# Kernel tuning notes

Hardware: AMD Instinct MI355X
Metric: run time of the kernel (lower is better)

Reference implementation:

```python
import jax, jax.numpy as jnp
import numpy as np

N, P, C, H, W, M = 2, 3, 80, 64, 64, 524288
HID = 64
BOX_WARP = 2.0


def _linear_init(key, fan_in, fan_out):
    # kaiming-uniform-ish; bias is zero-init per the torch module
    bound = 1.0 / np.sqrt(fan_in)
    return jax.random.uniform(key, (fan_in, fan_out), jnp.float32, -bound, bound)


def setup_inputs() -> dict:
    key = jax.random.key(0)
    ks = jax.random.split(key, 6)
    planes = jax.random.normal(ks[0], (N, P, C, H, W), jnp.float32)
    coordinates = jax.random.uniform(ks[1], (N, M, 3), jnp.float32, -1.0, 1.0)
    W1 = _linear_init(ks[2], 3 * C, HID)
    W2 = _linear_init(ks[3], HID, HID)
    W3 = _linear_init(ks[4], HID, HID)
    W4 = _linear_init(ks[5], HID, 1)
    return {
        "planes": planes, "coordinates": coordinates,
        "W1": W1, "b1": jnp.zeros((HID,), jnp.float32),
        "W2": W2, "b2": jnp.zeros((HID,), jnp.float32),
        "W3": W3, "b3": jnp.zeros((HID,), jnp.float32),
        "W4": W4, "b4": jnp.zeros((1,), jnp.float32),
    }


def _grid_sample_bilinear(feat, grid):
    # feat: [B, C, H, W]; grid: [B, M, 2] in [-1, 1] (x, y order),
    # bilinear, padding_mode='zeros', align_corners=False (matches torch).
    B, Cc, Hh, Ww = feat.shape
    gx = (grid[..., 0] + 1.0) * (Ww * 0.5) - 0.5  # [B, M]
    gy = (grid[..., 1] + 1.0) * (Hh * 0.5) - 0.5
    x0 = jnp.floor(gx)
    y0 = jnp.floor(gy)
    wx1 = gx - x0
    wy1 = gy - y0
    featf = feat.transpose(0, 2, 3, 1).reshape(B, Hh * Ww, Cc)  # [B, HW, C]

    def gather(xi, yi):
        valid = (xi >= 0) & (xi < Ww) & (yi >= 0) & (yi < Hh)
        xc = jnp.clip(xi, 0, Ww - 1).astype(jnp.int32)
        yc = jnp.clip(yi, 0, Hh - 1).astype(jnp.int32)
        idx = yc * Ww + xc  # [B, M]
        v = jnp.take_along_axis(featf, idx[..., None], axis=1)  # [B, M, C]
        return v * valid[..., None].astype(feat.dtype)

    v00 = gather(x0, y0)
    v01 = gather(x0 + 1, y0)
    v10 = gather(x0, y0 + 1)
    v11 = gather(x0 + 1, y0 + 1)
    wx1 = wx1[..., None]
    wy1 = wy1[..., None]
    top = v00 * (1.0 - wx1) + v01 * wx1
    bot = v10 * (1.0 - wx1) + v11 * wx1
    return top * (1.0 - wy1) + bot * wy1  # [B, M, C]


def _plane_axes():
    return jnp.array(
        [[[1, 0, 0], [0, 1, 0], [0, 0, 1]],
         [[1, 0, 0], [0, 0, 1], [0, 1, 0]],
         [[0, 0, 1], [0, 1, 0], [1, 0, 0]]], jnp.float32)


def reference(planes, coordinates, W1, b1, W2, b2, W3, b3, W4, b4):
    n, p, c, h, w = planes.shape
    m = coordinates.shape[1]
    inv_axes = jnp.linalg.inv(_plane_axes())  # [3, 3, 3]
    coords = (2.0 / BOX_WARP) * coordinates  # [N, M, 3]
    # project: coords @ inv_plane per plane, keep first two coords
    proj = jnp.einsum('nmc,pcd->npmd', coords, inv_axes)[..., :2]  # [N, P, M, 2]
    feat = planes.reshape(n * p, c, h, w)
    grid = proj.reshape(n * p, m, 2)
    samp = _grid_sample_bilinear(feat, grid)  # [N*P, M, C]
    # [N, P, M, C] -> [N, M, P*C]
    x = samp.reshape(n, p, m, c).transpose(0, 2, 1, 3).reshape(n, m, p * c)
    hdn = jax.nn.relu(x @ W1 + b1)
    hdn = jax.nn.relu(hdn @ W2 + b2)
    hdn = jax.nn.relu(hdn @ W3 + b3)
    sdf = hdn @ W4 + b4  # [N, M, 1]
    return sdf
```

## Files before the change

kernel.cpp:

```cpp
#include <hip/hip_runtime.h>
#include <hip/hip_bf16.h>
#include <stdint.h>

#define MPTS  524288
#define NB    2
#define CCH   80
#define HWDIM 64
#define HID   64

typedef _Float16 f16x2 __attribute__((ext_vector_type(2)));
typedef _Float16 f16x8 __attribute__((ext_vector_type(8)));
typedef float    f32x4 __attribute__((ext_vector_type(4)));

union FragH { uint4 q; f16x8 v; f16x2 h2[4]; _Float16 h[8]; };

__device__ __forceinline__ void fma_mix_lo(float& acc, unsigned u, float w) {
    asm volatile("v_fma_mix_f32 %0, %1, %2, %0 op_sel_hi:[1,0,0]"
                 : "+v"(acc) : "v"(u), "v"(w));
}
__device__ __forceinline__ void fma_mix_hi(float& acc, unsigned u, float w) {
    asm volatile("v_fma_mix_f32 %0, %1, %2, %0 op_sel:[1,0,0] op_sel_hi:[1,0,0]"
                 : "+v"(acc) : "v"(u), "v"(w));
}

__global__ void precompute_planesW(const float* __restrict__ planes,
                                   const float* __restrict__ W1,
                                   unsigned short* __restrict__ planesW) {
    __shared__ float tA[CCH * 64];
    __shared__ float tW[CCH * 64];
    int b  = blockIdx.x;
    int np = b >> 6, y = b & 63;
    int p  = np % 3;
    int t  = threadIdx.x;
    for (int i = t; i < CCH * 64; i += 256) {
        int c = i >> 6, x = i & 63;
        tA[i] = planes[((size_t)np * CCH + c) * 4096 + y * 64 + x];
        tW[i] = W1[(p * CCH + c) * HID + x];
    }
    __syncthreads();
    int px = t >> 2;
    int n0 = (t & 3) * 16;
    float acc[16];
    #pragma unroll
    for (int i = 0; i < 16; ++i) acc[i] = 0.0f;
    for (int c = 0; c < CCH; ++c) {
        float a = tA[c * 64 + px];
        #pragma unroll
        for (int i = 0; i < 16; ++i) acc[i] += a * tW[c * 64 + n0 + i];
    }
    unsigned short* dst = planesW + (((size_t)np * 4096) + y * 64 + px) * HID + n0;
    #pragma unroll
    for (int i = 0; i < 16; ++i) {
        union { _Float16 h; unsigned short u; } cv;
        cv.h = (_Float16)acc[i];
        dst[i] = cv.u;
    }
}

__global__ void pack_weights23(const float* __restrict__ W2,
                               const float* __restrict__ W3,
                               unsigned short* __restrict__ wpack) {
    int e = blockIdx.x * 256 + threadIdx.x;
    const float* W = (e < 4096) ? W2 : W3;
    int q  = e & 4095;
    int j  = q & 7;
    int l  = (q >> 3) & 63;
    int nt = (q >> 9) & 3;
    int kb = q >> 11;
    int k  = kb * 32 + ((l >> 4) << 3) + j;
    int nn = nt * 16 + (l & 15);
    union { _Float16 h; unsigned short u; } cv;
    cv.h = (_Float16)W[k * HID + nn];
    wpack[e] = cv.u;
}

__global__ __launch_bounds__(256, 4) void fused_kernel(
        const unsigned short* __restrict__ planesW,
        const float* __restrict__ coords,
        const unsigned short* __restrict__ wpack,
        const float* __restrict__ b1, const float* __restrict__ b2,
        const float* __restrict__ b3, const float* __restrict__ W4,
        const float* __restrict__ b4, float* __restrict__ out) {

    __shared__ __align__(16) unsigned short sH[4 * 16 * 72];
    __shared__ __align__(16) uint4 sSet[64][3][2];

    int t    = threadIdx.x;
    int wave = t >> 6, lane = t & 63;
    int ptbase = blockIdx.x * 64 + wave * 16;

    unsigned short* hw = sH + wave * (16 * 72);
    _Float16* hwh = (_Float16*)hw;

    if (t < 192) {
        int i  = t & 63;
        int p  = t >> 6;
        int mypt = blockIdx.x * 64 + i;
        int n    = mypt >> 19;
        const float* cp = coords + (size_t)mypt * 3;
        float c0 = cp[0], c1 = cp[1], c2 = cp[2];
        float gx = (p == 2) ? c2 : c0;
        float gy = (p == 1) ? c2 : c1;
        float fx = (gx + 1.0f) * 32.0f - 0.5f;
        float fy = (gy + 1.0f) * 32.0f - 0.5f;
        float xf = floorf(fx), yf = floorf(fy);
        float wx = fx - xf,    wy = fy - yf;
        int x0 = (int)xf, y0 = (int)yf, x1 = x0 + 1, y1 = y0 + 1;
        float vx0 = (x0 >= 0 && x0 < 64) ? 1.0f : 0.0f;
        float vx1 = (x1 >= 0 && x1 < 64) ? 1.0f : 0.0f;
        float vy0 = (y0 >= 0 && y0 < 64) ? 1.0f : 0.0f;
        float vy1 = (y1 >= 0 && y1 < 64) ? 1.0f : 0.0f;
        int cx0 = min(max(x0, 0), 63), cx1 = min(max(x1, 0), 63);
        int cy0 = min(max(y0, 0), 63), cy1 = min(max(y1, 0), 63);
        union { float f[4]; uint4 q; } wq;
        wq.f[0] = (1.0f - wx) * (1.0f - wy) * vx0 * vy0;
        wq.f[1] = wx * (1.0f - wy) * vx1 * vy0;
        wq.f[2] = (1.0f - wx) * wy * vx0 * vy1;
        wq.f[3] = wx * wy * vx1 * vy1;
        int base = (n * 3 + p) * 4096;
        uint4 oq;
        oq.x = (unsigned)((base + (cy0 << 6) + cx0) * HID);
        oq.y = (unsigned)((base + (cy0 << 6) + cx1) * HID);
        oq.z = (unsigned)((base + (cy1 << 6) + cx0) * HID);
        oq.w = (unsigned)((base + (cy1 << 6) + cx1) * HID);
        sSet[i][p][0] = oq;
        sSet[i][p][1] = wq.q;
    }
    __syncthreads();

    {
        int sub = lane & 7;
        int ptg = lane >> 3;

        float b1f0, b1f1, b1f2, b1f3, b1f4, b1f5, b1f6, b1f7;
        {
            const float4* bp = (const float4*)(b1 + sub * 8);
            float4 v0 = bp[0], v1 = bp[1];
            b1f0 = v0.x; b1f1 = v0.y; b1f2 = v0.z; b1f3 = v0.w;
            b1f4 = v1.x; b1f5 = v1.y; b1f6 = v1.z; b1f7 = v1.w;
        }
        const unsigned short* pw = planesW + sub * 8;

        auto do_round = [&](int pt) {
            int pl = wave * 16 + pt;
            uint4 o0 = sSet[pl][0][0], w0c = sSet[pl][0][1];
            uint4 o1 = sSet[pl][1][0], w1c = sSet[pl][1][1];
            uint4 o2 = sSet[pl][2][0], w2c = sSet[pl][2][1];

            FragH u0, u1, u2, u3, u4, u5, u6, u7, u8, u9, u10, u11;
            u0.q  = *(const uint4*)(pw + o0.x);
            u1.q  = *(const uint4*)(pw + o0.y);
            u2.q  = *(const uint4*)(pw + o0.z);
            u3.q  = *(const uint4*)(pw + o0.w);
            u4.q  = *(const uint4*)(pw + o1.x);
            u5.q  = *(const uint4*)(pw + o1.y);
            u6.q  = *(const uint4*)(pw + o1.z);
            u7.q  = *(const uint4*)(pw + o1.w);
            u8.q  = *(const uint4*)(pw + o2.x);
            u9.q  = *(const uint4*)(pw + o2.y);
            u10.q = *(const uint4*)(pw + o2.z);
            u11.q = *(const uint4*)(pw + o2.w);

            float a0 = b1f0, a1 = b1f1, a2 = b1f2, a3 = b1f3;
            float a4 = b1f4, a5 = b1f5, a6 = b1f6, a7 = b1f7;
            union { unsigned u; float f; } cvu;

            #define TEXEL(T, WB) { cvu.u = (WB); float w = cvu.f;            \
                fma_mix_lo(a0, T.q.x, w); fma_mix_hi(a1, T.q.x, w);          \
                fma_mix_lo(a2, T.q.y, w); fma_mix_hi(a3, T.q.y, w);          \
                fma_mix_lo(a4, T.q.z, w); fma_mix_hi(a5, T.q.z, w);          \
                fma_mix_lo(a6, T.q.w, w); fma_mix_hi(a7, T.q.w, w); }
            TEXEL(u0,  w0c.x) TEXEL(u1,  w0c.y) TEXEL(u2,  w0c.z) TEXEL(u3,  w0c.w)
            TEXEL(u4,  w1c.x) TEXEL(u5,  w1c.y) TEXEL(u6,  w1c.z) TEXEL(u7,  w1c.w)
            TEXEL(u8,  w2c.x) TEXEL(u9,  w2c.y) TEXEL(u10, w2c.z) TEXEL(u11, w2c.w)
            #undef TEXEL

            FragH hv;
            hv.h[0] = (_Float16)fmaxf(a0, 0.0f);
            hv.h[1] = (_Float16)fmaxf(a1, 0.0f);
            hv.h[2] = (_Float16)fmaxf(a2, 0.0f);
            hv.h[3] = (_Float16)fmaxf(a3, 0.0f);
            hv.h[4] = (_Float16)fmaxf(a4, 0.0f);
            hv.h[5] = (_Float16)fmaxf(a5, 0.0f);
            hv.h[6] = (_Float16)fmaxf(a6, 0.0f);
            hv.h[7] = (_Float16)fmaxf(a7, 0.0f);
            *(uint4*)(hwh + pt * 72 + sub * 8) = hv.q;
        };
        do_round(ptg);
        do_round(8 + ptg);
    }
    __syncthreads();

    int row  = lane & 15;
    int kgrp = lane >> 4;
    f32x4 acc2[4] = {{0,0,0,0},{0,0,0,0},{0,0,0,0},{0,0,0,0}};
    #pragma unroll
    for (int kk = 0; kk < 2; ++kk) {
        FragH au;
        au.q = *(const uint4*)(hw + row * 72 + kk * 32 + kgrp * 8);
        #pragma unroll
        for (int nt = 0; nt < 4; ++nt) {
            FragH bu;
            bu.q = *(const uint4*)(wpack + (kk * 4 + nt) * 512 + lane * 8);
            acc2[nt] = __builtin_amdgcn_mfma_f32_16x16x32_f16(au.v, bu.v, acc2[nt], 0, 0, 0);
        }
    }
    __syncthreads();

    #pragma unroll
    for (int nt = 0; nt < 4; ++nt) {
        float bb = b2[nt * 16 + row];
        #pragma unroll
        for (int r = 0; r < 4; ++r) {
            float h = fmaxf(acc2[nt][r] + bb, 0.0f);
            hwh[(kgrp * 4 + r) * 72 + nt * 16 + row] = (_Float16)h;
        }
    }
    __syncthreads();

    f32x4 acc3[4] = {{0,0,0,0},{0,0,0,0},{0,0,0,0},{0,0,0,0}};
    #pragma unroll
    for (int kk = 0; kk < 2; ++kk) {
        FragH au;
        au.q = *(const uint4*)(hw + row * 72 + kk * 32 + kgrp * 8);
        #pragma unroll
        for (int nt = 0; nt < 4; ++nt) {
            FragH bu;
            bu.q = *(const uint4*)(wpack + 4096 + (kk * 4 + nt) * 512 + lane * 8);
            acc3[nt] = __builtin_amdgcn_mfma_f32_16x16x32_f16(au.v, bu.v, acc3[nt], 0, 0, 0);
        }
    }

    float part[4] = {0.f, 0.f, 0.f, 0.f};
    #pragma unroll
    for (int nt = 0; nt < 4; ++nt) {
        float bb  = b3[nt * 16 + row];
        float w4v = W4[nt * 16 + row];
        #pragma unroll
        for (int r = 0; r < 4; ++r) {
            float h = fmaxf(acc3[nt][r] + bb, 0.0f);
            part[r] += h * w4v;
        }
    }
    #pragma unroll
    for (int r = 0; r < 4; ++r) {
        #pragma unroll
        for (int off = 1; off < 16; off <<= 1)
            part[r] += __shfl_xor(part[r], off);
    }
    if (row == 0) {
        float bias4 = b4[0];
        float4 o;
        o.x = part[0] + bias4; o.y = part[1] + bias4;
        o.z = part[2] + bias4; o.w = part[3] + bias4;
        *(float4*)(out + ptbase + kgrp * 4) = o;
    }
}

extern "C" void kernel_launch(void* const* d_in, const int* in_sizes, int n_in,
                              void* d_out, int out_size, void* d_ws, size_t ws_size,
                              hipStream_t stream) {
    const float* planes = (const float*)d_in[0];
    const float* coords = (const float*)d_in[1];
    const float* W1 = (const float*)d_in[2];
    const float* b1 = (const float*)d_in[3];
    const float* W2 = (const float*)d_in[4];
    const float* b2 = (const float*)d_in[5];
    const float* W3 = (const float*)d_in[6];
    const float* b3 = (const float*)d_in[7];
    const float* W4 = (const float*)d_in[8];
    const float* b4 = (const float*)d_in[9];
    float* out = (float*)d_out;

    unsigned short* planesW = (unsigned short*)d_ws;
    unsigned short* wpack   = (unsigned short*)((char*)d_ws + 3145728);

    hipLaunchKernelGGL(precompute_planesW, dim3(NB * 3 * HWDIM), dim3(256), 0, stream,
                       planes, W1, planesW);
    hipLaunchKernelGGL(pack_weights23, dim3(32), dim3(256), 0, stream,
                       W2, W3, wpack);

    int nblocks = (NB * MPTS) / 64;
    hipLaunchKernelGGL(fused_kernel, dim3(nblocks), dim3(256), 0, stream,
                       planesW, coords, wpack, b1, b2, b3, W4, b4, out);
}
```

Before: 108.4 us.

## Sort points into spatial cells before fused gather-MLP kernel for cache locality

Adds a counting sort of the 1M query points into 16x16x16 spatial cells per batch (histogram with atomics, single-block scan, atomic scatter into a permutation). The fused kernel reads points through the permutation and scatters outputs back to their original positions. The aim is for nearby points in a block to gather nearby texels of the precomputed plane features, improving L2/L1 hit rates. The cost is three extra kernels plus a memset, atomic contention, and scattered 4-byte output stores instead of float4 stores.

```diff
diff --git a/kernel.cpp b/kernel.cpp
--- a/kernel.cpp
+++ b/kernel.cpp
@@ -7,6 +7,8 @@
 #define CCH   80
 #define HWDIM 64
 #define HID   64
+#define NPTS  (NB * MPTS)
+#define NCELL 8192
 
 typedef _Float16 f16x2 __attribute__((ext_vector_type(2)));
 typedef _Float16 f16x8 __attribute__((ext_vector_type(8)));
@@ -21,6 +23,50 @@
 __device__ __forceinline__ void fma_mix_hi(float& acc, unsigned u, float w) {
     asm volatile("v_fma_mix_f32 %0, %1, %2, %0 op_sel:[1,0,0] op_sel_hi:[1,0,0]"
                  : "+v"(acc) : "v"(u), "v"(w));
+}
+
+__device__ __forceinline__ int cell_key(const float* __restrict__ coords, int idx) {
+    const float* cp = coords + (size_t)idx * 3;
+    int cx = min(max((int)((cp[0] + 1.0f) * 8.0f), 0), 15);
+    int cy = min(max((int)((cp[1] + 1.0f) * 8.0f), 0), 15);
+    int cz = min(max((int)((cp[2] + 1.0f) * 8.0f), 0), 15);
+    return ((idx >> 19) << 12) | (cx << 8) | (cy << 4) | cz;
+}
+
+__global__ void hist_kernel(const float* __restrict__ coords,
+                            unsigned* __restrict__ hist) {
+    int idx = blockIdx.x * 256 + threadIdx.x;
+    if (idx >= NPTS) return;
+    atomicAdd(&hist[cell_key(coords, idx)], 1u);
+}
+
+__global__ __launch_bounds__(1024) void scan_kernel(unsigned* __restrict__ hist) {
+    __shared__ unsigned s[1024];
+    int t = threadIdx.x;
+    unsigned v[8], pre[8], sum = 0;
+    #pragma unroll
+    for (int j = 0; j < 8; ++j) { v[j] = hist[t * 8 + j]; pre[j] = sum; sum += v[j]; }
+    s[t] = sum;
+    __syncthreads();
+    for (int off = 1; off < 1024; off <<= 1) {
+        unsigned x = 0;
+        if (t >= off) x = s[t - off];
+        __syncthreads();
+        if (t >= off) s[t] += x;
+        __syncthreads();
+    }
+    unsigned base = (t > 0) ? s[t - 1] : 0u;
+    #pragma unroll
+    for (int j = 0; j < 8; ++j) hist[t * 8 + j] = base + pre[j];
+}
+
+__global__ void scatter_kernel(const float* __restrict__ coords,
+                               unsigned* __restrict__ cursor,
+                               unsigned* __restrict__ perm) {
+    int idx = blockIdx.x * 256 + threadIdx.x;
+    if (idx >= NPTS) return;
+    unsigned slot = atomicAdd(&cursor[cell_key(coords, idx)], 1u);
+    perm[slot] = (unsigned)idx;
 }
 
 __global__ void precompute_planesW(const float* __restrict__ planes,
@@ -77,6 +123,7 @@
 __global__ __launch_bounds__(256, 4) void fused_kernel(
         const unsigned short* __restrict__ planesW,
         const float* __restrict__ coords,
+        const unsigned* __restrict__ perm,
         const unsigned short* __restrict__ wpack,
         const float* __restrict__ b1, const float* __restrict__ b2,
         const float* __restrict__ b3, const float* __restrict__ W4,
@@ -84,10 +131,10 @@
 
     __shared__ __align__(16) unsigned short sH[4 * 16 * 72];
     __shared__ __align__(16) uint4 sSet[64][3][2];
+    __shared__ unsigned sPermL[64];
 
     int t    = threadIdx.x;
     int wave = t >> 6, lane = t & 63;
-    int ptbase = blockIdx.x * 64 + wave * 16;
 
     unsigned short* hw = sH + wave * (16 * 72);
     _Float16* hwh = (_Float16*)hw;
@@ -95,8 +142,9 @@
     if (t < 192) {
         int i  = t & 63;
         int p  = t >> 6;
-        int mypt = blockIdx.x * 64 + i;
-        int n    = mypt >> 19;
+        unsigned mypt = perm[blockIdx.x * 64 + i];
+        if (t < 64) sPermL[i] = mypt;
+        int n = (int)(mypt >> 19);
         const float* cp = coords + (size_t)mypt * 3;
         float c0 = cp[0], c1 = cp[1], c2 = cp[2];
         float gx = (p == 2) ? c2 : c0;
@@ -250,10 +298,9 @@
     }
     if (row == 0) {
         float bias4 = b4[0];
-        float4 o;
-        o.x = part[0] + bias4; o.y = part[1] + bias4;
-        o.z = part[2] + bias4; o.w = part[3] + bias4;
-        *(float4*)(out + ptbase + kgrp * 4) = o;
+        #pragma unroll
+        for (int r = 0; r < 4; ++r)
+            out[sPermL[wave * 16 + kgrp * 4 + r]] = part[r] + bias4;
     }
 }
 
@@ -274,13 +321,22 @@
 
     unsigned short* planesW = (unsigned short*)d_ws;
     unsigned short* wpack   = (unsigned short*)((char*)d_ws + 3145728);
+    unsigned*       cursor  = (unsigned*)((char*)d_ws + 3162112);
+    unsigned*       perm    = (unsigned*)((char*)d_ws + 3194880);
+
+    hipMemsetAsync(cursor, 0, NCELL * sizeof(unsigned), stream);
+    hipLaunchKernelGGL(hist_kernel, dim3(NPTS / 256), dim3(256), 0, stream,
+                       coords, cursor);
+    hipLaunchKernelGGL(scan_kernel, dim3(1), dim3(1024), 0, stream, cursor);
+    hipLaunchKernelGGL(scatter_kernel, dim3(NPTS / 256), dim3(256), 0, stream,
+                       coords, cursor, perm);
 
     hipLaunchKernelGGL(precompute_planesW, dim3(NB * 3 * HWDIM), dim3(256), 0, stream,
                        planes, W1, planesW);
     hipLaunchKernelGGL(pack_weights23, dim3(32), dim3(256), 0, stream,
                        W2, W3, wpack);
 
-    int nblocks = (NB * MPTS) / 64;
+    int nblocks = NPTS / 64;
     hipLaunchKernelGGL(fused_kernel, dim3(nblocks), dim3(256), 0, stream,
-                       planesW, coords, wpack, b1, b2, b3, W4, b4, out);
-}
+                       planesW, coords, perm, wpack, b1, b2, b3, W4, b4, out);
+}
```

New measurement: 261.6 us. 141% more time.
